# Kernel optimization log

Measured on AMD Instinct MI355X. Metric: run time of the kernel, lower is better.

Reference implementation:

```python
import jax, jax.numpy as jnp
import numpy as np

V, E, H, L, C = 50257, 256, 256, 2, 64
B, T = 4, 48
MASK_ID = 103
EPS = 1e-5
SAMPLE_KEY = jax.random.key(1234)


def lstm_cell(x, h, c, Wih, Whh, bih, bhh):
    # PyTorch gate order: i, f, g, o
    z = x @ Wih.T + h @ Whh.T + (bih + bhh)  # [B,4H]
    i, f, g, o = jnp.split(z, 4, axis=-1)
    c = jax.nn.sigmoid(f) * c + jax.nn.sigmoid(i) * jnp.tanh(g)
    h = jax.nn.sigmoid(o) * jnp.tanh(c)
    return h, c


def setup_inputs() -> dict:
    key = jax.random.key(0)
    ks = jax.random.split(key, 16)
    g = lambda k, s: (jax.random.normal(k, s, dtype=jnp.float32) * 0.05)
    emb = g(ks[0], (V, E)).at[0].set(0.0)  # padding_idx=0 row zeroed
    params = dict(
        emb=emb,
        W_e2e=g(ks[1], (H, E)), b_e2e=jnp.zeros((H,), jnp.float32),
        W_e2d=g(ks[2], (H, E)), b_e2d=jnp.zeros((H,), jnp.float32),
        enc_Wih=g(ks[3], (L, 4 * H, H)), enc_Whh=g(ks[4], (L, 4 * H, H)),
        enc_bih=jnp.zeros((L, 4 * H), jnp.float32), enc_bhh=jnp.zeros((L, 4 * H), jnp.float32),
        dec_Wih=g(ks[5], (L, 4 * H, H)), dec_Whh=g(ks[6], (L, 4 * H, H)),
        dec_bih=jnp.zeros((L, 4 * H), jnp.float32), dec_bhh=jnp.zeros((L, 4 * H), jnp.float32),
        W_cls=g(ks[7], (C, 1)), b_cls=jnp.zeros((C,), jnp.float32),
        W_fc1=g(ks[8], (H + C, H + C)), b_fc1=jnp.zeros((H + C,), jnp.float32),
        ln_g=jnp.ones((H + C,), jnp.float32), ln_b=jnp.zeros((H + C,), jnp.float32),
        W_fc2=g(ks[9], (V, H + C)), b_fc2=jnp.zeros((V,), jnp.float32),
    )
    input_ids = jax.random.randint(ks[10], (B, T), 0, V, dtype=jnp.int32)
    mask_pos = jax.random.bernoulli(ks[11], 0.3, (B, T))  # ensure masked slots exist
    input_ids = jnp.where(mask_pos, jnp.int32(MASK_ID), input_ids)
    attention_mask = jnp.ones((B, T), jnp.int32)
    classification_labels = jax.random.bernoulli(ks[12], 0.5, (B,)).astype(jnp.float32)
    return dict(input_ids=input_ids, attention_mask=attention_mask,
                classification_labels=classification_labels, **params)


def _forward(input_ids, classification_labels, emb, W_e2e, b_e2e, W_e2d, b_e2d,
             enc_Wih, enc_Whh, enc_bih, enc_bhh, dec_Wih, dec_Whh, dec_bih, dec_bhh,
             W_cls, b_cls, W_fc1, b_fc1, ln_g, ln_b, W_fc2, b_fc2):
    f32 = jnp.float32
    # ---- encoder: embed -> linear+relu (dropout=eval identity) -> 2-layer LSTM ----
    xe = jax.nn.relu(emb[input_ids] @ W_e2e.T + b_e2e)  # [B,T,H]
    xs = jnp.swapaxes(xe, 0, 1)  # [T,B,H]
    h0 = jnp.zeros((L, B, H), f32)

    def enc_step(hc, xj):
        h, c = hc
        cur, hs, cs = xj, [], []
        for l in range(L):
            nh, nc = lstm_cell(cur, h[l], c[l], enc_Wih[l], enc_Whh[l], enc_bih[l], enc_bhh[l])
            hs.append(nh); cs.append(nc); cur = nh
        return (jnp.stack(hs), jnp.stack(cs)), None

    (h, c), _ = jax.lax.scan(enc_step, (h0, h0), xs)

    # classifier states are loop-invariant in the original (hoisted, same math)
    cls_states = classification_labels[:, None] @ W_cls.T + b_cls  # [B,C]

    tokens0 = jnp.zeros((B, T), input_ids.dtype).at[:, 0].set(input_ids[:, 0])

    def decode_step(carry, t):
        tokens, h, c = carry
        # re-embed the ENTIRE current prefix, as the original does each step
        x = jax.nn.relu(emb[tokens] @ W_e2d.T + b_e2d)  # [B,T,H]
        xs_t = jnp.swapaxes(x, 0, 1)  # [T,B,H]

        def mstep(hc, inp):
            hh, cc = hc
            xj, j = inp
            cur, hs, cs = xj, [], []
            for l in range(L):
                nh, nc = lstm_cell(cur, hh[l], cc[l], dec_Wih[l], dec_Whh[l], dec_bih[l], dec_bhh[l])
                hs.append(nh); cs.append(nc); cur = nh
            nh, nc = jnp.stack(hs), jnp.stack(cs)
            valid = j < t  # only positions 0..t-1 are real prefix tokens
            hh = jnp.where(valid, nh, hh)
            cc = jnp.where(valid, nc, cc)
            return (hh, cc), hh[-1]

        (h, c), ys = jax.lax.scan(mstep, (h, c), (xs_t, jnp.arange(T)))
        dec_out = jax.lax.dynamic_index_in_dim(ys, t - 1, axis=0, keepdims=False)  # [B,H]

        z = jnp.concatenate([dec_out, cls_states], axis=-1)  # [B,H+C]
        z1 = jax.nn.relu(z @ W_fc1.T + b_fc1)
        mu = z1.mean(-1, keepdims=True)
        var = ((z1 - mu) ** 2).mean(-1, keepdims=True)
        z1 = (z1 - mu) * jax.lax.rsqrt(var + EPS) * ln_g + ln_b
        logits = z1 @ W_fc2.T + b_fc2  # [B,V]
        logp = jax.nn.log_softmax(logits, axis=-1)

        gumb = jax.random.gumbel(jax.random.fold_in(SAMPLE_KEY, t), logp.shape)
        sampled = jnp.argmax(logp + gumb, axis=-1)  # [B] categorical sample
        slp = jnp.take_along_axis(logp, sampled[:, None], axis=-1)[:, 0]  # [B]

        cur_tok = jnp.take(input_ids, t, axis=1)  # [B]
        next_tok = jnp.where(cur_tok == MASK_ID, sampled.astype(tokens.dtype), cur_tok)
        tokens = jax.lax.dynamic_update_slice(tokens, next_tok[:, None], (0, t))
        return (tokens, h, c), slp

    (tokens, h, c), slps = jax.lax.scan(decode_step, (tokens0, h, c), jnp.arange(1, T))
    scores = jnp.concatenate([jnp.zeros((B, 1), f32), slps.T], axis=1)  # [B,T]
    return scores, tokens


def reference(input_ids, attention_mask, classification_labels, emb, W_e2e, b_e2e,
              W_e2d, b_e2d, enc_Wih, enc_Whh, enc_bih, enc_bhh, dec_Wih, dec_Whh,
              dec_bih, dec_bhh, W_cls, b_cls, W_fc1, b_fc1, ln_g, ln_b, W_fc2, b_fc2):
    # attention_mask is accepted but unused, matching the original forward
    return _forward(input_ids, classification_labels, emb, W_e2e, b_e2e, W_e2d, b_e2d,
                    enc_Wih, enc_Whh, enc_bih, enc_bhh, dec_Wih, dec_Whh, dec_bih, dec_bhh,
                    W_cls, b_cls, W_fc1, b_fc1, ln_g, ln_b, W_fc2, b_fc2)
```

## Files before the change

### kernel.cpp

```cpp
#include <hip/hip_runtime.h>
#include <stdint.h>
#include <stddef.h>
#include <math.h>


#define PARTITIONABLE_PRNG 1

namespace s2sr {

constexpr int kV = 50257, kE = 256, kH = 256, kCc = 64, kB = 4, kT = 48;
constexpr int kZ = kH + kCc;
constexpr int kG = 4 * kH;
constexpr int kMask = 103;
constexpr float kEps = 1e-5f;
constexpr float kTiny = 1.17549435e-38f;

constexpr int NWG = 256, TPB = 256;
constexpr int NCL = 32;
constexpr int LEAD = 32;
constexpr int GANG0 = 33;
constexpr int NGANG = NWG - GANG0;
constexpr int RPW = (kV + NGANG - 1) / NGANG;
constexpr int NPX = 16;

constexpr int SH_H0 = 0;
constexpr int SH_H1 = 1024;
constexpr int SH_P0 = 2048;
constexpr int SH_P1 = 3072;
constexpr int SH_Z  = 4096;
constexpr int SH_TOT = 4608;
constexpr int LD_ZIN = 0;
constexpr int LD_Z1  = 1280;
constexpr int LD_CLS = 2560;
constexpr int LD_LSE = 2816;
constexpr int LD_WPS = 2820;

struct alignas(128) Tag { unsigned v; unsigned _p[31]; };
struct alignas(128) GOut {
  unsigned long long key[kB];
  float ps[kB];
  unsigned tag;
  unsigned _p[19];
};

struct SyncBlk {
  Tag ictr, igen;
  Tag ptok4[NPX][4];
  Tag ztag4[4];
  Tag etok4[4];
  Tag hztag[NCL];
  GOut gout[NGANG];
};

struct WS {
  SyncBlk s;
  unsigned long long hc[2][2][NCL][32];
  float hzbuf[2][kB][kH];
  float z1n[2][kB][kZ];
  float xcur[kB][kH];
  float xd0[kB][kH];
  float px0[kT][kB][kG];
  float pxe[kT][kB][kG];
};

__device__ __forceinline__ float aldf(const float* p) {
  return __hip_atomic_load(p, __ATOMIC_RELAXED, __HIP_MEMORY_SCOPE_AGENT);
}
__device__ __forceinline__ void astf(float* p, float v) {
  __hip_atomic_store(p, v, __ATOMIC_RELAXED, __HIP_MEMORY_SCOPE_AGENT);
}
__device__ __forceinline__ unsigned ldu(const unsigned* p) {
  return __hip_atomic_load(p, __ATOMIC_RELAXED, __HIP_MEMORY_SCOPE_AGENT);
}
__device__ __forceinline__ unsigned long long ld64(const unsigned long long* p) {
  return __hip_atomic_load(p, __ATOMIC_RELAXED, __HIP_MEMORY_SCOPE_AGENT);
}
__device__ __forceinline__ void st64(unsigned long long* p, unsigned long long v) {
  __hip_atomic_store(p, v, __ATOMIC_RELAXED, __HIP_MEMORY_SCOPE_AGENT);
}
__device__ __forceinline__ void relTag(Tag* tg, unsigned v) {
  __hip_atomic_store(&tg->v, v, __ATOMIC_RELEASE, __HIP_MEMORY_SCOPE_AGENT);
}
__device__ __forceinline__ void gbar(SyncBlk* sb, unsigned tgt) {
  __syncthreads();
  if (threadIdx.x == 0) {
    const unsigned old = __hip_atomic_fetch_add(&sb->ictr.v, 1u, __ATOMIC_RELEASE,
                                                __HIP_MEMORY_SCOPE_AGENT);
    if (old == tgt - 1u) relTag(&sb->igen, tgt);
    while (ldu(&sb->igen.v) < tgt) __builtin_amdgcn_s_sleep(2);
    __atomic_signal_fence(__ATOMIC_ACQUIRE);
  }
  __syncthreads();
}

__device__ __forceinline__ unsigned rotl32(unsigned v, int n) {
  return (v << n) | (v >> (32 - n));
}
__device__ __forceinline__ void tf2x32(unsigned k0, unsigned k1, unsigned x0, unsigned x1,
                                       unsigned& o0, unsigned& o1) {
  const unsigned k2 = k0 ^ k1 ^ 0x1BD11BDAu;
  unsigned v0 = x0 + k0, v1 = x1 + k1;
  v0 += v1; v1 = rotl32(v1, 13); v1 ^= v0;
  v0 += v1; v1 = rotl32(v1, 15); v1 ^= v0;
  v0 += v1; v1 = rotl32(v1, 26); v1 ^= v0;
  v0 += v1; v1 = rotl32(v1, 6);  v1 ^= v0;
  v0 += k1; v1 += k2 + 1u;
  v0 += v1; v1 = rotl32(v1, 17); v1 ^= v0;
  v0 += v1; v1 = rotl32(v1, 29); v1 ^= v0;
  v0 += v1; v1 = rotl32(v1, 16); v1 ^= v0;
  v0 += v1; v1 = rotl32(v1, 24); v1 ^= v0;
  v0 += k2; v1 += k0 + 2u;
  v0 += v1; v1 = rotl32(v1, 13); v1 ^= v0;
  v0 += v1; v1 = rotl32(v1, 15); v1 ^= v0;
  v0 += v1; v1 = rotl32(v1, 26); v1 ^= v0;
  v0 += v1; v1 = rotl32(v1, 6);  v1 ^= v0;
  v0 += k0; v1 += k1 + 3u;
  v0 += v1; v1 = rotl32(v1, 17); v1 ^= v0;
  v0 += v1; v1 = rotl32(v1, 29); v1 ^= v0;
  v0 += v1; v1 = rotl32(v1, 16); v1 ^= v0;
  v0 += v1; v1 = rotl32(v1, 24); v1 ^= v0;
  v0 += k1; v1 += k2 + 4u;
  v0 += v1; v1 = rotl32(v1, 13); v1 ^= v0;
  v0 += v1; v1 = rotl32(v1, 15); v1 ^= v0;
  v0 += v1; v1 = rotl32(v1, 26); v1 ^= v0;
  v0 += v1; v1 = rotl32(v1, 6);  v1 ^= v0;
  o0 = v0 + k2; o1 = v1 + k0 + 5u;
}
__device__ __forceinline__ unsigned rbits(unsigned k0, unsigned k1, unsigned i) {
#if PARTITIONABLE_PRNG
  unsigned a, b; tf2x32(k0, k1, 0u, i, a, b);
  return a ^ b;
#else
  constexpr unsigned HALF = (unsigned)((kB * kV + 1) / 2);
  unsigned a, b;
  if (i < HALF) { tf2x32(k0, k1, i, i + HALF, a, b); return a; }
  tf2x32(k0, k1, i - HALF, i, a, b); return b;
#endif
}
__device__ __forceinline__ float gumbel_from_bits(unsigned bits) {
  float f = __uint_as_float((bits >> 9) | 0x3f800000u) - 1.0f;
  f = fmaxf(f, kTiny);
  return -logf(-logf(f));
}
__device__ __forceinline__ unsigned ordkey(float f) {
  const unsigned u = __float_as_uint(f);
  return (u & 0x80000000u) ? ~u : (u | 0x80000000u);
}
__device__ __forceinline__ unsigned long long shflx64(unsigned long long v, int m) {
  unsigned lo = (unsigned)v, hi = (unsigned)(v >> 32);
  lo = (unsigned)__shfl_xor((int)lo, m, 64);
  hi = (unsigned)__shfl_xor((int)hi, m, 64);
  return ((unsigned long long)hi << 32) | (unsigned long long)lo;
}
__device__ __forceinline__ float sigm(float x) { return 1.0f / (1.0f + expf(-x)); }

template <bool STREAM>
__device__ __forceinline__ void lstm_tick(
    WS* ws, float* shf, int cw, int cc, bool do_l0, bool do_l1,
    const float* px, const float* pW0, const float* pW1,
    const float4* w0r, const float4* w1r, float biasr,
    float& c0, float& c1, float& h0last, float& h1last,
    int grow, int r, int w, int hzt) {
  const int tid = (int)threadIdx.x;
  float pxv0 = 0.f, pxv1 = 0.f, pxv2 = 0.f, pxv3 = 0.f;
  if (do_l0 && tid < 32) {
    pxv0 = aldf(px + 0 * kG + grow);
    pxv1 = aldf(px + 1 * kG + grow);
    pxv2 = aldf(px + 2 * kG + grow);
    pxv3 = aldf(px + 3 * kG + grow);
  }
  {
    const unsigned long long* base = &ws->hc[(cc + 1) & 1][0][0][0];
    const unsigned exp = (unsigned)cc;
    unsigned long long v[8];
#pragma unroll
    for (int k = 0; k < 8; ++k) v[k] = ld64(base + tid * 8 + k);
    unsigned pend = 0;
#pragma unroll
    for (int k = 0; k < 8; ++k) if ((unsigned)v[k] != exp) pend |= 1u << k;
    while (pend) {
#pragma unroll
      for (int k = 0; k < 8; ++k)
        if (pend & (1u << k)) v[k] = ld64(base + tid * 8 + k);
#pragma unroll
      for (int k = 0; k < 8; ++k)
        if ((unsigned)v[k] == exp) pend &= ~(1u << k);
    }
#pragma unroll
    for (int k = 0; k < 8; ++k) {
      const int c = tid * 8 + k, L = c >> 10, rem = c & 1023;
      const int wg2 = rem >> 5, s = rem & 31;
      shf[L * 1024 + (s >> 3) * 256 + wg2 * 8 + (s & 7)] =
          __uint_as_float((unsigned)(v[k] >> 32));
    }
  }
  __syncthreads();
  float4 wv0[8], wv1[16];
  if (do_l0) {
#pragma unroll
    for (int i = 0; i < 8; ++i)
      wv0[i] = STREAM ? *reinterpret_cast<const float4*>(pW0 + i * 4) : w0r[i];
  }
  if (do_l1) {
#pragma unroll
    for (int i = 0; i < 16; ++i)
      wv1[i] = STREAM ? *reinterpret_cast<const float4*>(pW1 + i * 4) : w1r[i];
  }
  if (do_l0) {
    const float* A = &shf[SH_H0 + w * 32];
    float a0 = 0.f, a1 = 0.f, a2 = 0.f, a3 = 0.f;
#pragma unroll
    for (int i = 0; i < 8; ++i) {
      const float4 wv = wv0[i];
      const float4 x0 = *reinterpret_cast<const float4*>(A + 0 * 256 + i * 4);
      const float4 x1 = *reinterpret_cast<const float4*>(A + 1 * 256 + i * 4);
      const float4 x2 = *reinterpret_cast<const float4*>(A + 2 * 256 + i * 4);
      const float4 x3 = *reinterpret_cast<const float4*>(A + 3 * 256 + i * 4);
      a0 = fmaf(wv.x, x0.x, a0); a0 = fmaf(wv.y, x0.y, a0); a0 = fmaf(wv.z, x0.z, a0); a0 = fmaf(wv.w, x0.w, a0);
      a1 = fmaf(wv.x, x1.x, a1); a1 = fmaf(wv.y, x1.y, a1); a1 = fmaf(wv.z, x1.z, a1); a1 = fmaf(wv.w, x1.w, a1);
      a2 = fmaf(wv.x, x2.x, a2); a2 = fmaf(wv.y, x2.y, a2); a2 = fmaf(wv.z, x2.z, a2); a2 = fmaf(wv.w, x2.w, a2);
      a3 = fmaf(wv.x, x3.x, a3); a3 = fmaf(wv.y, x3.y, a3); a3 = fmaf(wv.z, x3.z, a3); a3 = fmaf(wv.w, x3.w, a3);
    }
    *reinterpret_cast<float4*>(&shf[SH_P0 + w * 128 + r * 4]) = float4{a0, a1, a2, a3};
  }
  if (do_l1) {
    const float* Bp = (w < 4) ? &shf[SH_H0 + w * 64] : &shf[SH_H1 + (w - 4) * 64];
    float a0 = 0.f, a1 = 0.f, a2 = 0.f, a3 = 0.f;
#pragma unroll
    for (int i = 0; i < 16; ++i) {
      const float4 wv = wv1[i];
      const float4 x0 = *reinterpret_cast<const float4*>(Bp + 0 * 256 + i * 4);
      const float4 x1 = *reinterpret_cast<const float4*>(Bp + 1 * 256 + i * 4);
      const float4 x2 = *reinterpret_cast<const float4*>(Bp + 2 * 256 + i * 4);
      const float4 x3 = *reinterpret_cast<const float4*>(Bp + 3 * 256 + i * 4);
      a0 = fmaf(wv.x, x0.x, a0); a0 = fmaf(wv.y, x0.y, a0); a0 = fmaf(wv.z, x0.z, a0); a0 = fmaf(wv.w, x0.w, a0);
      a1 = fmaf(wv.x, x1.x, a1); a1 = fmaf(wv.y, x1.y, a1); a1 = fmaf(wv.z, x1.z, a1); a1 = fmaf(wv.w, x1.w, a1);
      a2 = fmaf(wv.x, x2.x, a2); a2 = fmaf(wv.y, x2.y, a2); a2 = fmaf(wv.z, x2.z, a2); a2 = fmaf(wv.w, x2.w, a2);
      a3 = fmaf(wv.x, x3.x, a3); a3 = fmaf(wv.y, x3.y, a3); a3 = fmaf(wv.z, x3.z, a3); a3 = fmaf(wv.w, x3.w, a3);
    }
    *reinterpret_cast<float4*>(&shf[SH_P1 + w * 128 + r * 4]) = float4{a0, a1, a2, a3};
  }
  __syncthreads();
  if (tid < 64) {
    const int L = tid >> 5, rr = tid & 31;
    const bool en = L ? do_l1 : do_l0;
    if (en) {
      const int base = (L ? SH_P1 : SH_P0) + rr * 4;
      float4 z = float4{0.f, 0.f, 0.f, 0.f};
#pragma unroll
      for (int w2 = 0; w2 < 8; ++w2) {
        const float4 p = *reinterpret_cast<const float4*>(&shf[base + w2 * 128]);
        z.x += p.x; z.y += p.y; z.z += p.z; z.w += p.w;
      }
      z.x += biasr; z.y += biasr; z.z += biasr; z.w += biasr;
      if (L == 0) { z.x += pxv0; z.y += pxv1; z.z += pxv2; z.w += pxv3; }
      *reinterpret_cast<float4*>(&shf[SH_Z + L * 128 + rr * 4]) = z;
    }
  }
  __syncthreads();
  if (tid < 64) {
    const int L = tid >> 5, slot = tid & 31, b = slot >> 3, u = slot & 7;
    const bool en = L ? do_l1 : do_l0;
    float hn;
    if (en) {
      const int zb = SH_Z + L * 128 + u * 16 + b;
      const float zi = shf[zb], zf = shf[zb + 4], zg = shf[zb + 8], zo = shf[zb + 12];
      const float cs = L ? c1 : c0;
      const float cn = sigm(zf) * cs + sigm(zi) * tanhf(zg);
      hn = sigm(zo) * tanhf(cn);
      if (L) c1 = cn; else c0 = cn;
    } else {
      hn = L ? h1last : h0last;
    }
    if (L) h1last = hn; else h0last = hn;
    st64(&ws->hc[cc & 1][L][cw][slot],
         ((unsigned long long)__float_as_uint(hn) << 32) |
         (unsigned long long)(unsigned)(cc + 1));
    if (L && hzt >= 0) astf(&ws->hzbuf[hzt & 1][b][cw * 8 + u], hn);
  }
}

__global__ void __launch_bounds__(TPB, 1) s2s_kernel(
    const int* __restrict__ input_ids, const float* __restrict__ labels,
    const float* __restrict__ emb,
    const float* __restrict__ W_e2e, const float* __restrict__ b_e2e,
    const float* __restrict__ W_e2d, const float* __restrict__ b_e2d,
    const float* __restrict__ encWih, const float* __restrict__ encWhh,
    const float* __restrict__ encbih, const float* __restrict__ encbhh,
    const float* __restrict__ decWih, const float* __restrict__ decWhh,
    const float* __restrict__ decbih, const float* __restrict__ decbhh,
    const float* __restrict__ W_cls, const float* __restrict__ b_cls,
    const float* __restrict__ Wfc1, const float* __restrict__ bfc1,
    const float* __restrict__ lng, const float* __restrict__ lnb,
    const float* __restrict__ W_fc2, const float* __restrict__ b_fc2,
    float* __restrict__ out, WS* __restrict__ ws) {
  const int wg = (int)blockIdx.x;
  const int tid = (int)threadIdx.x;
  SyncBlk* sb = &ws->s;
  __shared__ __align__(16) float shf[SH_TOT];
  __shared__ unsigned long long shk[16];
  __shared__ int shi[8];

  if (wg < kB * kT) {
    const int b = wg / kT, j = wg % kT;
    const int id = input_ids[b * kT + j];
    for (int i = tid; i < kE; i += 256) shf[i] = emb[(size_t)id * kE + i];
    __syncthreads();
    const float* wr = W_e2e + (size_t)tid * kE;
    float acc = b_e2e[tid];
    for (int k = 0; k < kE; k += 4) {
      const float4 wv = *reinterpret_cast<const float4*>(wr + k);
      const float4 xv = *reinterpret_cast<const float4*>(&shf[k]);
      acc = fmaf(xv.x, wv.x, acc); acc = fmaf(xv.y, wv.y, acc);
      acc = fmaf(xv.z, wv.z, acc); acc = fmaf(xv.w, wv.w, acc);
    }
    __syncthreads();
    shf[256 + tid] = fmaxf(acc, 0.f);
  } else if (wg == 192) {
    if (tid < kB) {
      const int t0 = input_ids[tid * kT];
      out[tid * kT] = 0.f;
      out[kB * kT + tid * kT] = (float)t0;
    }
  } else if (wg == 193) {
    const float* wr = W_e2d + (size_t)tid * kE;
    const float* e0 = emb + (size_t)input_ids[0 * kT] * kE;
    const float* e1 = emb + (size_t)input_ids[1 * kT] * kE;
    const float* e2 = emb + (size_t)input_ids[2 * kT] * kE;
    const float* e3 = emb + (size_t)input_ids[3 * kT] * kE;
    const float bb = b_e2d[tid];
    float a0 = bb, a1 = bb, a2 = bb, a3 = bb;
    for (int k = 0; k < kE; k += 4) {
      const float4 wv = *reinterpret_cast<const float4*>(wr + k);
      const float4 v0 = *reinterpret_cast<const float4*>(e0 + k);
      const float4 v1 = *reinterpret_cast<const float4*>(e1 + k);
      const float4 v2 = *reinterpret_cast<const float4*>(e2 + k);
      const float4 v3 = *reinterpret_cast<const float4*>(e3 + k);
      a0 = fmaf(v0.x, wv.x, a0); a0 = fmaf(v0.y, wv.y, a0); a0 = fmaf(v0.z, wv.z, a0); a0 = fmaf(v0.w, wv.w, a0);
      a1 = fmaf(v1.x, wv.x, a1); a1 = fmaf(v1.y, wv.y, a1); a1 = fmaf(v1.z, wv.z, a1); a1 = fmaf(v1.w, wv.w, a1);
      a2 = fmaf(v2.x, wv.x, a2); a2 = fmaf(v2.y, wv.y, a2); a2 = fmaf(v2.z, wv.z, a2); a2 = fmaf(v2.w, wv.w, a2);
      a3 = fmaf(v3.x, wv.x, a3); a3 = fmaf(v3.y, wv.y, a3); a3 = fmaf(v3.z, wv.z, a3); a3 = fmaf(v3.w, wv.w, a3);
    }
    astf(&ws->xd0[0][tid], fmaxf(a0, 0.f));
    astf(&ws->xd0[1][tid], fmaxf(a1, 0.f));
    astf(&ws->xd0[2][tid], fmaxf(a2, 0.f));
    astf(&ws->xd0[3][tid], fmaxf(a3, 0.f));
  }
  gbar(sb, (unsigned)NWG);

  if (wg < kB * kT) {
    const int b = wg / kT, j = wg % kT;
#pragma unroll
    for (int rr = 0; rr < 4; ++rr) {
      const int g = rr * 256 + tid;
      const float* wr = encWih + (size_t)g * kH;
      float acc = 0.f;
      for (int k = 0; k < kH; k += 4) {
        const float4 wv = *reinterpret_cast<const float4*>(wr + k);
        const float4 xv = *reinterpret_cast<const float4*>(&shf[256 + k]);
        acc = fmaf(xv.x, wv.x, acc); acc = fmaf(xv.y, wv.y, acc);
        acc = fmaf(xv.z, wv.z, acc); acc = fmaf(xv.w, wv.w, acc);
      }
      astf(&ws->pxe[j][0][0] + (size_t)b * kG + g, acc);
    }
  } else if (wg >= 192 && wg < 208) {
    const int w2 = wg - 192, b = w2 >> 2, q = w2 & 3;
    const int g = q * 256 + tid;
    for (int i = tid; i < kH; i += 256) shf[i] = aldf(&ws->xd0[b][i]);
    __syncthreads();
    const float* wr = decWih + (size_t)g * kH;
    float acc = 0.f;
    for (int k = 0; k < kH; k += 4) {
      const float4 wv = *reinterpret_cast<const float4*>(wr + k);
      const float4 xv = *reinterpret_cast<const float4*>(&shf[k]);
      acc = fmaf(xv.x, wv.x, acc); acc = fmaf(xv.y, wv.y, acc);
      acc = fmaf(xv.z, wv.z, acc); acc = fmaf(xv.w, wv.w, acc);
    }
    astf(&ws->px0[0][0][0] + (size_t)b * kG + g, acc);
  }
  gbar(sb, (unsigned)(2 * NWG));

  if (wg < NCL) {
    const int cw = wg;
    const int r = tid & 31, w = tid >> 5;
    const int grow = (r & 3) * 256 + cw * 8 + (r >> 2);
    const int L = tid >> 5;
    float c0 = 0.f, c1 = 0.f, h0last = 0.f, h1last = 0.f;
    float biasr = 0.f;
    if (tid < 64)
      biasr = (L == 0) ? encbih[grow] + encbhh[grow]
                       : encbih[kG + grow] + encbhh[kG + grow];
    const float* pW0e = encWhh + (size_t)grow * kH + w * 32;
    const float* pW1e = (w < 4)
        ? encWih + (size_t)kG * kH + (size_t)grow * kH + w * 64
        : encWhh + (size_t)kG * kH + (size_t)grow * kH + (w - 4) * 64;
    int cc = 0;
    for (int j = 0; j < kT; ++j, ++cc)
      lstm_tick<true>(ws, shf, cw, cc, true, j > 0, &ws->pxe[j][0][0],
                      pW0e, pW1e, nullptr, nullptr, biasr, c0, c1,
                      h0last, h1last, grow, r, w, -1);
    lstm_tick<true>(ws, shf, cw, cc, false, true, nullptr,
                    pW0e, pW1e, nullptr, nullptr, biasr, c0, c1,
                    h0last, h1last, grow, r, w, -1);
    ++cc;
    float4 w0d[8], w1d[16];
    {
      const float* p0 = decWhh + (size_t)grow * kH + w * 32;
#pragma unroll
      for (int i = 0; i < 8; ++i) w0d[i] = *reinterpret_cast<const float4*>(p0 + i * 4);
      const float* p1 = (w < 4)
          ? decWih + (size_t)kG * kH + (size_t)grow * kH + w * 64
          : decWhh + (size_t)kG * kH + (size_t)grow * kH + (w - 4) * 64;
#pragma unroll
      for (int i = 0; i < 16; ++i) w1d[i] = *reinterpret_cast<const float4*>(p1 + i * 4);
      if (tid < 64)
        biasr = (L == 0) ? decbih[grow] + decbhh[grow]
                         : decbih[kG + grow] + decbhh[kG + grow];
    }
    for (int t = 1; t < kT; ++t) {
      for (int j = 0; j < t; ++j, ++cc) {
        const bool d1 = (j > 0) || (t >= 2);
        const int hzt = (j == 0 && t >= 2) ? (t - 1) : -1;
        if (j == t - 1 && t >= 2) {
          if (tid < 64) {
            Tag* p = &sb->ptok4[tid >> 2][tid & 3];
            while (ldu(&p->v) < (unsigned)(t - 1)) {}
            __atomic_signal_fence(__ATOMIC_ACQUIRE);
          }
          __syncthreads();
        }
        lstm_tick<false>(ws, shf, cw, cc, true, d1, &ws->px0[j][0][0],
                         nullptr, nullptr, w0d, w1d, biasr, c0, c1,
                         h0last, h1last, grow, r, w, hzt);
        if (hzt >= 0 && tid == 0) relTag(&sb->hztag[cw], (unsigned)hzt);
      }
    }
    lstm_tick<false>(ws, shf, cw, cc, false, true, nullptr,
                     nullptr, nullptr, w0d, w1d, biasr, c0, c1,
                     h0last, h1last, grow, r, w, kT - 1);
    if (tid == 0) relTag(&sb->hztag[cw], (unsigned)(kT - 1));
  } else if (wg == LEAD) {
    if (tid < kB * kCc) {
      const int b = tid >> 6, c = tid & 63;
      shf[LD_CLS + tid] = fmaf(labels[b], W_cls[c], b_cls[c]);
    }
    __syncthreads();
    for (int t = 1; t < kT; ++t) {
      if (tid < NCL) {
        while (ldu(&sb->hztag[tid].v) < (unsigned)t) __builtin_amdgcn_s_sleep(1);
        __atomic_signal_fence(__ATOMIC_ACQUIRE);
      }
      __syncthreads();
      for (int i = tid; i < kB * kZ; i += 256) {
        const int b = i / kZ, k = i - b * kZ;
        shf[LD_ZIN + i] = (k < kH) ? aldf(&ws->hzbuf[t & 1][b][k])
                                   : shf[LD_CLS + b * kCc + (k - kH)];
      }
      __syncthreads();
#pragma unroll
      for (int rep = 0; rep < 5; ++rep) {
        const int task = tid + rep * 256;
        const int b = task / kZ, o = task - b * kZ;
        const float* wr = Wfc1 + (size_t)o * kZ;
        const float* zz = &shf[LD_ZIN + b * kZ];
        float acc = bfc1[o];
        for (int k = 0; k < kZ; k += 4) {
          const float4 wv = *reinterpret_cast<const float4*>(wr + k);
          const float4 zv = *reinterpret_cast<const float4*>(zz + k);
          acc = fmaf(zv.x, wv.x, acc); acc = fmaf(zv.y, wv.y, acc);
          acc = fmaf(zv.z, wv.z, acc); acc = fmaf(zv.w, wv.w, acc);
        }
        shf[LD_Z1 + task] = fmaxf(acc, 0.f);
      }
      __syncthreads();
      {
        const int b = tid >> 6, ln = tid & 63;
        float s1 = 0.f, s2 = 0.f;
        for (int i = ln; i < kZ; i += 64) {
          const float v = shf[LD_Z1 + b * kZ + i]; s1 += v; s2 += v * v;
        }
#pragma unroll
        for (int o = 32; o > 0; o >>= 1) { s1 += __shfl_xor(s1, o, 64); s2 += __shfl_xor(s2, o, 64); }
        const float mu = s1 * (1.0f / kZ);
        const float var = s2 * (1.0f / kZ) - mu * mu;
        const float rs = 1.0f / sqrtf(var + kEps);
        for (int i = ln; i < kZ; i += 64) {
          const float v = fmaf((shf[LD_Z1 + b * kZ + i] - mu) * rs, lng[i], lnb[i]);
          shf[LD_Z1 + b * kZ + i] = v;
          astf(&ws->z1n[t & 1][b][i], v);
        }
        if (ln == 0) relTag(&sb->ztag4[b], (unsigned)t);
      }
      if (tid < NGANG) {
        while (ldu(&sb->gout[tid].tag) < (unsigned)t) __builtin_amdgcn_s_sleep(2);
        __atomic_signal_fence(__ATOMIC_ACQUIRE);
      }
      __syncthreads();
      {
        unsigned long long kk[kB];
        float pp[kB];
        if (tid < NGANG) {
          const GOut* g = &sb->gout[tid];
#pragma unroll
          for (int b = 0; b < kB; ++b) { kk[b] = ld64(&g->key[b]); pp[b] = aldf(&g->ps[b]); }
        } else {
#pragma unroll
          for (int b = 0; b < kB; ++b) { kk[b] = 0ull; pp[b] = 0.f; }
        }
#pragma unroll
        for (int b = 0; b < kB; ++b) {
#pragma unroll
          for (int m = 1; m < 64; m <<= 1) {
            const unsigned long long ko = shflx64(kk[b], m);
            pp[b] += __shfl_xor(pp[b], m, 64);
            if (ko > kk[b]) kk[b] = ko;
          }
        }
        if ((tid & 63) == 0) {
          const int wv = tid >> 6;
#pragma unroll
          for (int b = 0; b < kB; ++b) { shk[wv * kB + b] = kk[b]; shf[LD_WPS + wv * kB + b] = pp[b]; }
        }
      }
      __syncthreads();
      if (tid < kB) {
        const int b = tid;
        unsigned long long key = shk[b];
        float s = shf[LD_WPS + b];
        for (int wv = 1; wv < 4; ++wv) {
          const unsigned long long ko = shk[wv * kB + b];
          if (ko > key) key = ko;
          s += shf[LD_WPS + wv * kB + b];
        }
        const int samp = (int)(0xFFFFFFFFu - (unsigned)(key & 0xFFFFFFFFull));
        const float lse = logf(s);
        const int cur = input_ids[b * kT + t];
        const int nxt = (cur == kMask) ? samp : cur;
        out[kB * kT + b * kT + t] = (float)nxt;
        shi[b] = nxt; shi[4 + b] = samp;
        shf[LD_LSE + b] = lse;
      }
      __syncthreads();
      if (t < kT - 1) {
        const float* wr = W_e2d + (size_t)tid * kE;
        const float* e0 = emb + (size_t)shi[0] * kE;
        const float* e1 = emb + (size_t)shi[1] * kE;
        const float* e2 = emb + (size_t)shi[2] * kE;
        const float* e3 = emb + (size_t)shi[3] * kE;
        const float bb = b_e2d[tid];
        float a0 = bb, a1 = bb, a2 = bb, a3 = bb;
        for (int k = 0; k < kE; k += 4) {
          const float4 wv = *reinterpret_cast<const float4*>(wr + k);
          const float4 v0 = *reinterpret_cast<const float4*>(e0 + k);
          const float4 v1 = *reinterpret_cast<const float4*>(e1 + k);
          const float4 v2 = *reinterpret_cast<const float4*>(e2 + k);
          const float4 v3 = *reinterpret_cast<const float4*>(e3 + k);
          a0 = fmaf(v0.x, wv.x, a0); a0 = fmaf(v0.y, wv.y, a0); a0 = fmaf(v0.z, wv.z, a0); a0 = fmaf(v0.w, wv.w, a0);
          a1 = fmaf(v1.x, wv.x, a1); a1 = fmaf(v1.y, wv.y, a1); a1 = fmaf(v1.z, wv.z, a1); a1 = fmaf(v1.w, wv.w, a1);
          a2 = fmaf(v2.x, wv.x, a2); a2 = fmaf(v2.y, wv.y, a2); a2 = fmaf(v2.z, wv.z, a2); a2 = fmaf(v2.w, wv.w, a2);
          a3 = fmaf(v3.x, wv.x, a3); a3 = fmaf(v3.y, wv.y, a3); a3 = fmaf(v3.z, wv.z, a3); a3 = fmaf(v3.w, wv.w, a3);
        }
        astf(&ws->xcur[0][tid], fmaxf(a0, 0.f));
        astf(&ws->xcur[1][tid], fmaxf(a1, 0.f));
        astf(&ws->xcur[2][tid], fmaxf(a2, 0.f));
        astf(&ws->xcur[3][tid], fmaxf(a3, 0.f));
        if ((tid & 63) == 0) relTag(&sb->etok4[tid >> 6], (unsigned)t);
      }
      {
        const int b = tid >> 6, lane = tid & 63;
        const int sp = shi[4 + b];
        const float* wr = W_fc2 + (size_t)sp * kZ;
        float acc = 0.f;
#pragma unroll
        for (int i = 0; i < 5; ++i)
          acc = fmaf(shf[LD_Z1 + b * kZ + lane + i * 64], wr[lane + i * 64], acc);
#pragma unroll
        for (int o = 32; o > 0; o >>= 1) acc += __shfl_xor(acc, o, 64);
        if (lane == 0) out[b * kT + t] = acc + b_fc2[sp] - shf[LD_LSE + b];
      }
      __syncthreads();
    }
  } else {
    const int gi = wg - GANG0;
    const int start = gi * RPW;
    const int cnt = (RPW < kV - start) ? RPW : (kV - start);
    const bool act = tid < cnt;
    const int row = start + tid;
    for (int t = 1; t < kT; ++t) {
      if (tid < 4) {
        while (ldu(&sb->ztag4[tid].v) < (unsigned)t) __builtin_amdgcn_s_sleep(16);
        __atomic_signal_fence(__ATOMIC_ACQUIRE);
      }
      __syncthreads();
      for (int i = tid; i < kB * kZ; i += 256) shf[i] = aldf(&ws->z1n[t & 1][0][0] + i);
      __syncthreads();
      unsigned fk0, fk1;
      tf2x32(0u, 1234u, 0u, (unsigned)t, fk0, fk1);
      float lv[kB] = {0.f, 0.f, 0.f, 0.f};
      if (act) {
        const float* wr = W_fc2 + (size_t)row * kZ;
        const float bb = b_fc2[row];
        float a0 = bb, a1 = bb, a2 = bb, a3 = bb;
        for (int k = 0; k < kZ; k += 4) {
          const float4 wv = *reinterpret_cast<const float4*>(wr + k);
          const float4 z0 = *reinterpret_cast<const float4*>(&shf[0 * kZ + k]);
          const float4 z1 = *reinterpret_cast<const float4*>(&shf[1 * kZ + k]);
          const float4 z2 = *reinterpret_cast<const float4*>(&shf[2 * kZ + k]);
          const float4 z3 = *reinterpret_cast<const float4*>(&shf[3 * kZ + k]);
          a0 = fmaf(z0.x, wv.x, a0); a0 = fmaf(z0.y, wv.y, a0); a0 = fmaf(z0.z, wv.z, a0); a0 = fmaf(z0.w, wv.w, a0);
          a1 = fmaf(z1.x, wv.x, a1); a1 = fmaf(z1.y, wv.y, a1); a1 = fmaf(z1.z, wv.z, a1); a1 = fmaf(z1.w, wv.w, a1);
          a2 = fmaf(z2.x, wv.x, a2); a2 = fmaf(z2.y, wv.y, a2); a2 = fmaf(z2.z, wv.z, a2); a2 = fmaf(z2.w, wv.w, a2);
          a3 = fmaf(z3.x, wv.x, a3); a3 = fmaf(z3.y, wv.y, a3); a3 = fmaf(z3.z, wv.z, a3); a3 = fmaf(z3.w, wv.w, a3);
        }
        lv[0] = a0; lv[1] = a1; lv[2] = a2; lv[3] = a3;
      }
#pragma unroll
      for (int b = 0; b < kB; ++b) {
        unsigned long long key = 0ull;
        float sv = 0.f;
        if (act) {
          const unsigned bits = rbits(fk0, fk1, (unsigned)(b * kV + row));
          const float pv = lv[b] + gumbel_from_bits(bits);
          key = ((unsigned long long)ordkey(pv) << 32) |
                (unsigned long long)(0xFFFFFFFFu - (unsigned)row);
          sv = expf(lv[b]);
        }
#pragma unroll
        for (int m = 1; m < 64; m <<= 1) {
          const unsigned long long ko = shflx64(key, m);
          sv += __shfl_xor(sv, m, 64);
          if (ko > key) key = ko;
        }
        if ((tid & 63) == 0) { shk[(tid >> 6) * kB + b] = key; shf[1408 + (tid >> 6) * kB + b] = sv; }
      }
      __syncthreads();
      if (tid == 0) {
        GOut* g = &sb->gout[gi];
#pragma unroll
        for (int b = 0; b < kB; ++b) {
          unsigned long long key = shk[b];
          float s = shf[1408 + b];
          for (int w2 = 1; w2 < 4; ++w2) {
            const unsigned long long ko = shk[w2 * kB + b];
            if (ko > key) key = ko;
            s += shf[1408 + w2 * kB + b];
          }
          st64(&g->key[b], key);
          astf(&g->ps[b], s);
        }
        __hip_atomic_store(&g->tag, (unsigned)t, __ATOMIC_RELEASE, __HIP_MEMORY_SCOPE_AGENT);
      }
      __syncthreads();
      if (gi < NPX && t < kT - 1) {
        if (tid < 4) {
          while (ldu(&sb->etok4[tid].v) < (unsigned)t) __builtin_amdgcn_s_sleep(8);
          __atomic_signal_fence(__ATOMIC_ACQUIRE);
        }
        __syncthreads();
        for (int i = tid; i < kB * kH; i += 256) shf[i] = aldf(&ws->xcur[0][0] + i);
        __syncthreads();
        {
          const int rowg = gi * 64 + (tid & 63), b = tid >> 6;
          const float* wr = decWih + (size_t)rowg * kH;
          const float* xz = &shf[b * kH];
          float acc = 0.f;
          for (int k = 0; k < kH; k += 4) {
            const float4 wv = *reinterpret_cast<const float4*>(wr + k);
            const float4 xv = *reinterpret_cast<const float4*>(xz + k);
            acc = fmaf(xv.x, wv.x, acc); acc = fmaf(xv.y, wv.y, acc);
            acc = fmaf(xv.z, wv.z, acc); acc = fmaf(xv.w, wv.w, acc);
          }
          astf(&ws->px0[t][0][0] + (size_t)b * kG + rowg, acc);
          if ((tid & 63) == 0) relTag(&sb->ptok4[gi][tid >> 6], (unsigned)t);
        }
      }
      __syncthreads();
    }
  }
}

}

extern "C" void kernel_launch(void* const* d_in, const int* in_sizes, int n_in,
                              void* d_out, int out_size, void* d_ws, size_t ws_size,
                              hipStream_t stream) {
  using namespace s2sr;
  (void)in_sizes; (void)n_in; (void)out_size;
  if (ws_size < sizeof(WS)) return;
  const int*   input_ids = (const int*)d_in[0];
  const float* labels    = (const float*)d_in[2];
  const float* emb       = (const float*)d_in[3];
  const float* W_e2e     = (const float*)d_in[4];
  const float* b_e2e     = (const float*)d_in[5];
  const float* W_e2d     = (const float*)d_in[6];
  const float* b_e2d     = (const float*)d_in[7];
  const float* encWih    = (const float*)d_in[8];
  const float* encWhh    = (const float*)d_in[9];
  const float* encbih    = (const float*)d_in[10];
  const float* encbhh    = (const float*)d_in[11];
  const float* decWih    = (const float*)d_in[12];
  const float* decWhh    = (const float*)d_in[13];
  const float* decbih    = (const float*)d_in[14];
  const float* decbhh    = (const float*)d_in[15];
  const float* W_cls     = (const float*)d_in[16];
  const float* b_cls     = (const float*)d_in[17];
  const float* W_fc1     = (const float*)d_in[18];
  const float* b_fc1     = (const float*)d_in[19];
  const float* ln_g      = (const float*)d_in[20];
  const float* ln_b      = (const float*)d_in[21];
  const float* W_fc2     = (const float*)d_in[22];
  const float* b_fc2     = (const float*)d_in[23];

  hipMemsetAsync(d_ws, 0, (size_t)offsetof(WS, xd0), stream);
  hipLaunchKernelGGL(s2s_kernel, dim3(NWG), dim3(TPB), 0, stream,
      input_ids, labels, emb, W_e2e, b_e2e, W_e2d, b_e2d,
      encWih, encWhh, encbih, encbhh, decWih, decWhh, decbih, decbhh,
      W_cls, b_cls, W_fc1, b_fc1, ln_g, ln_b, W_fc2, b_fc2,
      (float*)d_out, (WS*)d_ws);
}
```

Before: 7.600 ms.

## Reduce LSTM gate partials with wave shuffles and drop per-tick block barriers

Each LSTM tick now maps gate rows so that one wavefront holds all eight k-slices of its rows. Partial dot products are combined with xor-shuffles and gathered into lanes that apply the cell update directly, replacing two shared-memory reduction stages and two __syncthreads per tick. The shared-memory staging buffer is double-buffered by tick parity so the next tick's writes do not race with the current reads. The hidden-state ready tag becomes per-wavefront, and the lead workgroup now polls 128 tags instead of 32. This trades more shuffle instructions and more tag polling for a shorter serial critical path in the recurrent loop.

```diff
diff --git a/kernel.cpp b/kernel.cpp
--- a/kernel.cpp
+++ b/kernel.cpp
@@ -23,11 +23,7 @@
 constexpr int RPW = (kV + NGANG - 1) / NGANG;
 constexpr int NPX = 16;
 
-constexpr int SH_H0 = 0;
-constexpr int SH_H1 = 1024;
-constexpr int SH_P0 = 2048;
-constexpr int SH_P1 = 3072;
-constexpr int SH_Z  = 4096;
+constexpr int SH_STG = 0;
 constexpr int SH_TOT = 4608;
 constexpr int LD_ZIN = 0;
 constexpr int LD_Z1  = 1280;
@@ -48,7 +44,7 @@
   Tag ptok4[NPX][4];
   Tag ztag4[4];
   Tag etok4[4];
-  Tag hztag[NCL];
+  Tag hztag[NCL][4];
   GOut gout[NGANG];
 };
 
@@ -156,58 +152,61 @@
 
 template <bool STREAM>
 __device__ __forceinline__ void lstm_tick(
-    WS* ws, float* shf, int cw, int cc, bool do_l0, bool do_l1,
+    WS* ws, float* shf, int cw, int cc, bool do0, bool do1,
     const float* px, const float* pW0, const float* pW1,
-    const float4* w0r, const float4* w1r, float biasr,
+    const float4* w0r, const float4* w1r,
+    const float* bs0, const float* bs1,
     float& c0, float& c1, float& h0last, float& h1last,
-    int grow, int r, int w, int hzt) {
+    int w, bool fin, int fu, int fb, int hzt) {
   const int tid = (int)threadIdx.x;
-  float pxv0 = 0.f, pxv1 = 0.f, pxv2 = 0.f, pxv3 = 0.f;
-  if (do_l0 && tid < 32) {
-    pxv0 = aldf(px + 0 * kG + grow);
-    pxv1 = aldf(px + 1 * kG + grow);
-    pxv2 = aldf(px + 2 * kG + grow);
-    pxv3 = aldf(px + 3 * kG + grow);
+  const int l = tid & 63;
+  const int par = cc & 1;
+  float pxg0 = 0.f, pxg1 = 0.f, pxg2 = 0.f, pxg3 = 0.f;
+  if (do0 && fin) {
+    const float* pb = px + fb * kG + cw * 8 + fu;
+    pxg0 = aldf(pb);
+    pxg1 = aldf(pb + 256);
+    pxg2 = aldf(pb + 512);
+    pxg3 = aldf(pb + 768);
   }
   {
     const unsigned long long* base = &ws->hc[(cc + 1) & 1][0][0][0];
-    const unsigned exp = (unsigned)cc;
+    const unsigned expseq = (unsigned)cc;
     unsigned long long v[8];
 #pragma unroll
-    for (int k = 0; k < 8; ++k) v[k] = ld64(base + tid * 8 + k);
+    for (int k = 0; k < 4; ++k) v[k] = ld64(base + tid * 4 + k);
+#pragma unroll
+    for (int k = 0; k < 4; ++k) v[4 + k] = ld64(base + 1024 + tid * 4 + k);
     unsigned pend = 0;
 #pragma unroll
-    for (int k = 0; k < 8; ++k) if ((unsigned)v[k] != exp) pend |= 1u << k;
+    for (int k = 0; k < 8; ++k) if ((unsigned)v[k] != expseq) pend |= 1u << k;
     while (pend) {
 #pragma unroll
       for (int k = 0; k < 8; ++k)
-        if (pend & (1u << k)) v[k] = ld64(base + tid * 8 + k);
+        if (pend & (1u << k))
+          v[k] = ld64(base + (k < 4 ? tid * 4 + k : 1024 + tid * 4 + (k - 4)));
 #pragma unroll
       for (int k = 0; k < 8; ++k)
-        if ((unsigned)v[k] == exp) pend &= ~(1u << k);
-    }
-#pragma unroll
-    for (int k = 0; k < 8; ++k) {
-      const int c = tid * 8 + k, L = c >> 10, rem = c & 1023;
-      const int wg2 = rem >> 5, s = rem & 31;
-      shf[L * 1024 + (s >> 3) * 256 + wg2 * 8 + (s & 7)] =
+        if ((unsigned)v[k] == expseq) pend &= ~(1u << k);
+    }
+#pragma unroll
+    for (int k = 0; k < 4; ++k) {
+      const int c = tid * 4 + k;
+      const int s = c & 31;
+      shf[SH_STG + par * 2048 + (s >> 3) * 256 + (c >> 5) * 8 + (s & 7)] =
           __uint_as_float((unsigned)(v[k] >> 32));
+      shf[SH_STG + par * 2048 + 1024 + (s >> 3) * 256 + (c >> 5) * 8 + (s & 7)] =
+          __uint_as_float((unsigned)(v[4 + k] >> 32));
     }
   }
   __syncthreads();
-  float4 wv0[8], wv1[16];
-  if (do_l0) {
+  float zl0[4] = {0.f, 0.f, 0.f, 0.f};
+  if (do0) {
+    float4 wv0[8];
 #pragma unroll
     for (int i = 0; i < 8; ++i)
       wv0[i] = STREAM ? *reinterpret_cast<const float4*>(pW0 + i * 4) : w0r[i];
-  }
-  if (do_l1) {
-#pragma unroll
-    for (int i = 0; i < 16; ++i)
-      wv1[i] = STREAM ? *reinterpret_cast<const float4*>(pW1 + i * 4) : w1r[i];
-  }
-  if (do_l0) {
-    const float* A = &shf[SH_H0 + w * 32];
+    const float* A = &shf[SH_STG + par * 2048 + w * 32];
     float a0 = 0.f, a1 = 0.f, a2 = 0.f, a3 = 0.f;
 #pragma unroll
     for (int i = 0; i < 8; ++i) {
@@ -221,10 +220,43 @@
       a2 = fmaf(wv.x, x2.x, a2); a2 = fmaf(wv.y, x2.y, a2); a2 = fmaf(wv.z, x2.z, a2); a2 = fmaf(wv.w, x2.w, a2);
       a3 = fmaf(wv.x, x3.x, a3); a3 = fmaf(wv.y, x3.y, a3); a3 = fmaf(wv.z, x3.z, a3); a3 = fmaf(wv.w, x3.w, a3);
     }
-    *reinterpret_cast<float4*>(&shf[SH_P0 + w * 128 + r * 4]) = float4{a0, a1, a2, a3};
-  }
-  if (do_l1) {
-    const float* Bp = (w < 4) ? &shf[SH_H0 + w * 64] : &shf[SH_H1 + (w - 4) * 64];
+#pragma unroll
+    for (int m = 1; m < 8; m <<= 1) {
+      a0 += __shfl_xor(a0, m, 64); a1 += __shfl_xor(a1, m, 64);
+      a2 += __shfl_xor(a2, m, 64); a3 += __shfl_xor(a3, m, 64);
+    }
+#pragma unroll
+    for (int g = 0; g < 4; ++g) {
+      const int src = ((((l & 7) >> 2) * 4) + g) * 8;
+      const float s0 = __shfl(a0, src, 64);
+      const float s1 = __shfl(a1, src, 64);
+      const float s2 = __shfl(a2, src, 64);
+      const float s3 = __shfl(a3, src, 64);
+      zl0[g] = (fb == 0) ? s0 : (fb == 1) ? s1 : (fb == 2) ? s2 : s3;
+    }
+  }
+  if (fin) {
+    if (do0) {
+      const float zi = zl0[0] + bs0[0] + pxg0;
+      const float zf = zl0[1] + bs0[1] + pxg1;
+      const float zg = zl0[2] + bs0[2] + pxg2;
+      const float zo = zl0[3] + bs0[3] + pxg3;
+      const float cn = sigm(zf) * c0 + sigm(zi) * tanhf(zg);
+      h0last = sigm(zo) * tanhf(cn);
+      c0 = cn;
+    }
+    st64(&ws->hc[cc & 1][0][cw][fb * 8 + fu],
+         ((unsigned long long)__float_as_uint(h0last) << 32) |
+         (unsigned long long)(unsigned)(cc + 1));
+  }
+  float zl1[4] = {0.f, 0.f, 0.f, 0.f};
+  if (do1) {
+    float4 wv1[16];
+#pragma unroll
+    for (int i = 0; i < 16; ++i)
+      wv1[i] = STREAM ? *reinterpret_cast<const float4*>(pW1 + i * 4) : w1r[i];
+    const float* Bp = (w < 4) ? &shf[SH_STG + par * 2048 + w * 64]
+                              : &shf[SH_STG + par * 2048 + 1024 + (w - 4) * 64];
     float a0 = 0.f, a1 = 0.f, a2 = 0.f, a3 = 0.f;
 #pragma unroll
     for (int i = 0; i < 16; ++i) {
@@ -238,45 +270,35 @@
       a2 = fmaf(wv.x, x2.x, a2); a2 = fmaf(wv.y, x2.y, a2); a2 = fmaf(wv.z, x2.z, a2); a2 = fmaf(wv.w, x2.w, a2);
       a3 = fmaf(wv.x, x3.x, a3); a3 = fmaf(wv.y, x3.y, a3); a3 = fmaf(wv.z, x3.z, a3); a3 = fmaf(wv.w, x3.w, a3);
     }
-    *reinterpret_cast<float4*>(&shf[SH_P1 + w * 128 + r * 4]) = float4{a0, a1, a2, a3};
-  }
-  __syncthreads();
-  if (tid < 64) {
-    const int L = tid >> 5, rr = tid & 31;
-    const bool en = L ? do_l1 : do_l0;
-    if (en) {
-      const int base = (L ? SH_P1 : SH_P0) + rr * 4;
-      float4 z = float4{0.f, 0.f, 0.f, 0.f};
-#pragma unroll
-      for (int w2 = 0; w2 < 8; ++w2) {
-        const float4 p = *reinterpret_cast<const float4*>(&shf[base + w2 * 128]);
-        z.x += p.x; z.y += p.y; z.z += p.z; z.w += p.w;
-      }
-      z.x += biasr; z.y += biasr; z.z += biasr; z.w += biasr;
-      if (L == 0) { z.x += pxv0; z.y += pxv1; z.z += pxv2; z.w += pxv3; }
-      *reinterpret_cast<float4*>(&shf[SH_Z + L * 128 + rr * 4]) = z;
-    }
-  }
-  __syncthreads();
-  if (tid < 64) {
-    const int L = tid >> 5, slot = tid & 31, b = slot >> 3, u = slot & 7;
-    const bool en = L ? do_l1 : do_l0;
-    float hn;
-    if (en) {
-      const int zb = SH_Z + L * 128 + u * 16 + b;
-      const float zi = shf[zb], zf = shf[zb + 4], zg = shf[zb + 8], zo = shf[zb + 12];
-      const float cs = L ? c1 : c0;
-      const float cn = sigm(zf) * cs + sigm(zi) * tanhf(zg);
-      hn = sigm(zo) * tanhf(cn);
-      if (L) c1 = cn; else c0 = cn;
-    } else {
-      hn = L ? h1last : h0last;
-    }
-    if (L) h1last = hn; else h0last = hn;
-    st64(&ws->hc[cc & 1][L][cw][slot],
-         ((unsigned long long)__float_as_uint(hn) << 32) |
+#pragma unroll
+    for (int m = 1; m < 8; m <<= 1) {
+      a0 += __shfl_xor(a0, m, 64); a1 += __shfl_xor(a1, m, 64);
+      a2 += __shfl_xor(a2, m, 64); a3 += __shfl_xor(a3, m, 64);
+    }
+#pragma unroll
+    for (int g = 0; g < 4; ++g) {
+      const int src = ((((l & 7) >> 2) * 4) + g) * 8;
+      const float s0 = __shfl(a0, src, 64);
+      const float s1 = __shfl(a1, src, 64);
+      const float s2 = __shfl(a2, src, 64);
+      const float s3 = __shfl(a3, src, 64);
+      zl1[g] = (fb == 0) ? s0 : (fb == 1) ? s1 : (fb == 2) ? s2 : s3;
+    }
+  }
+  if (fin) {
+    if (do1) {
+      const float zi = zl1[0] + bs1[0];
+      const float zf = zl1[1] + bs1[1];
+      const float zg = zl1[2] + bs1[2];
+      const float zo = zl1[3] + bs1[3];
+      const float cn = sigm(zf) * c1 + sigm(zi) * tanhf(zg);
+      h1last = sigm(zo) * tanhf(cn);
+      c1 = cn;
+    }
+    st64(&ws->hc[cc & 1][1][cw][fb * 8 + fu],
+         ((unsigned long long)__float_as_uint(h1last) << 32) |
          (unsigned long long)(unsigned)(cc + 1));
-    if (L && hzt >= 0) astf(&ws->hzbuf[hzt & 1][b][cw * 8 + u], hn);
+    if (hzt >= 0) astf(&ws->hzbuf[hzt & 1][fb][cw * 8 + fu], h1last);
   }
 }
 
@@ -382,14 +404,22 @@
 
   if (wg < NCL) {
     const int cw = wg;
-    const int r = tid & 31, w = tid >> 5;
+    const int v = tid >> 6, l = tid & 63;
+    const int r = v * 8 + (l >> 3);
+    const int w = l & 7;
     const int grow = (r & 3) * 256 + cw * 8 + (r >> 2);
-    const int L = tid >> 5;
+    const bool fin = l < 8;
+    const int fu = v * 2 + (l >> 2);
+    const int fb = l & 3;
     float c0 = 0.f, c1 = 0.f, h0last = 0.f, h1last = 0.f;
-    float biasr = 0.f;
-    if (tid < 64)
-      biasr = (L == 0) ? encbih[grow] + encbhh[grow]
-                       : encbih[kG + grow] + encbhh[kG + grow];
+    float bs0[4] = {0.f, 0.f, 0.f, 0.f}, bs1[4] = {0.f, 0.f, 0.f, 0.f};
+    if (fin) {
+#pragma unroll
+      for (int g = 0; g < 4; ++g) {
+        bs0[g] = encbih[g * 256 + cw * 8 + fu] + encbhh[g * 256 + cw * 8 + fu];
+        bs1[g] = encbih[kG + g * 256 + cw * 8 + fu] + encbhh[kG + g * 256 + cw * 8 + fu];
+      }
+    }
     const float* pW0e = encWhh + (size_t)grow * kH + w * 32;
     const float* pW1e = (w < 4)
         ? encWih + (size_t)kG * kH + (size_t)grow * kH + w * 64
@@ -397,11 +427,11 @@
     int cc = 0;
     for (int j = 0; j < kT; ++j, ++cc)
       lstm_tick<true>(ws, shf, cw, cc, true, j > 0, &ws->pxe[j][0][0],
-                      pW0e, pW1e, nullptr, nullptr, biasr, c0, c1,
-                      h0last, h1last, grow, r, w, -1);
+                      pW0e, pW1e, nullptr, nullptr, bs0, bs1,
+                      c0, c1, h0last, h1last, w, fin, fu, fb, -1);
     lstm_tick<true>(ws, shf, cw, cc, false, true, nullptr,
-                    pW0e, pW1e, nullptr, nullptr, biasr, c0, c1,
-                    h0last, h1last, grow, r, w, -1);
+                    pW0e, pW1e, nullptr, nullptr, bs0, bs1,
+                    c0, c1, h0last, h1last, w, fin, fu, fb, -1);
     ++cc;
     float4 w0d[8], w1d[16];
     {
@@ -413,9 +443,13 @@
           : decWhh + (size_t)kG * kH + (size_t)grow * kH + (w - 4) * 64;
 #pragma unroll
       for (int i = 0; i < 16; ++i) w1d[i] = *reinterpret_cast<const float4*>(p1 + i * 4);
-      if (tid < 64)
-        biasr = (L == 0) ? decbih[grow] + decbhh[grow]
-                         : decbih[kG + grow] + decbhh[kG + grow];
+      if (fin) {
+#pragma unroll
+        for (int g = 0; g < 4; ++g) {
+          bs0[g] = decbih[g * 256 + cw * 8 + fu] + decbhh[g * 256 + cw * 8 + fu];
+          bs1[g] = decbih[kG + g * 256 + cw * 8 + fu] + decbhh[kG + g * 256 + cw * 8 + fu];
+        }
+      }
     }
     for (int t = 1; t < kT; ++t) {
       for (int j = 0; j < t; ++j, ++cc) {
@@ -430,15 +464,15 @@
           __syncthreads();
         }
         lstm_tick<false>(ws, shf, cw, cc, true, d1, &ws->px0[j][0][0],
-                         nullptr, nullptr, w0d, w1d, biasr, c0, c1,
-                         h0last, h1last, grow, r, w, hzt);
-        if (hzt >= 0 && tid == 0) relTag(&sb->hztag[cw], (unsigned)hzt);
+                         nullptr, nullptr, w0d, w1d, bs0, bs1,
+                         c0, c1, h0last, h1last, w, fin, fu, fb, hzt);
+        if (hzt >= 0 && l == 0) relTag(&sb->hztag[cw][v], (unsigned)hzt);
       }
     }
     lstm_tick<false>(ws, shf, cw, cc, false, true, nullptr,
-                     nullptr, nullptr, w0d, w1d, biasr, c0, c1,
-                     h0last, h1last, grow, r, w, kT - 1);
-    if (tid == 0) relTag(&sb->hztag[cw], (unsigned)(kT - 1));
+                     nullptr, nullptr, w0d, w1d, bs0, bs1,
+                     c0, c1, h0last, h1last, w, fin, fu, fb, kT - 1);
+    if (l == 0) relTag(&sb->hztag[cw][v], (unsigned)(kT - 1));
   } else if (wg == LEAD) {
     if (tid < kB * kCc) {
       const int b = tid >> 6, c = tid & 63;
@@ -446,8 +480,9 @@
     }
     __syncthreads();
     for (int t = 1; t < kT; ++t) {
-      if (tid < NCL) {
-        while (ldu(&sb->hztag[tid].v) < (unsigned)t) __builtin_amdgcn_s_sleep(1);
+      if (tid < NCL * 4) {
+        while (ldu(&sb->hztag[tid >> 2][tid & 3].v) < (unsigned)t)
+          __builtin_amdgcn_s_sleep(1);
         __atomic_signal_fence(__ATOMIC_ACQUIRE);
       }
       __syncthreads();
@@ -477,7 +512,7 @@
         const int b = tid >> 6, ln = tid & 63;
         float s1 = 0.f, s2 = 0.f;
         for (int i = ln; i < kZ; i += 64) {
-          const float v = shf[LD_Z1 + b * kZ + i]; s1 += v; s2 += v * v;
+          const float v2 = shf[LD_Z1 + b * kZ + i]; s1 += v2; s2 += v2 * v2;
         }
 #pragma unroll
         for (int o = 32; o > 0; o >>= 1) { s1 += __shfl_xor(s1, o, 64); s2 += __shfl_xor(s2, o, 64); }
@@ -485,9 +520,9 @@
         const float var = s2 * (1.0f / kZ) - mu * mu;
         const float rs = 1.0f / sqrtf(var + kEps);
         for (int i = ln; i < kZ; i += 64) {
-          const float v = fmaf((shf[LD_Z1 + b * kZ + i] - mu) * rs, lng[i], lnb[i]);
-          shf[LD_Z1 + b * kZ + i] = v;
-          astf(&ws->z1n[t & 1][b][i], v);
+          const float v2 = fmaf((shf[LD_Z1 + b * kZ + i] - mu) * rs, lng[i], lnb[i]);
+          shf[LD_Z1 + b * kZ + i] = v2;
+          astf(&ws->z1n[t & 1][b][i], v2);
         }
         if (ln == 0) relTag(&sb->ztag4[b], (unsigned)t);
       }
```

New measurement: 10.45 ms. +37.5%, slower.
